# Kernel tuning notes

Hardware: AMD Instinct MI355X
Metric: run time of the kernel (lower is better)

## Reference

```python
import jax, jax.numpy as jnp
import numpy as np
from jax import lax

EPS = 1e-5


def _conv3x3(x, w):
    # NCHW input, OIHW weight, stride 1, padding 1
    return lax.conv_general_dilated(
        x, w, window_strides=(1, 1), padding=((1, 1), (1, 1)),
        dimension_numbers=("NCHW", "OIHW", "NCHW"))


def _batchnorm(y, gamma, beta):
    # training-mode BN: batch statistics over N,H,W
    mean = jnp.mean(y, axis=(0, 2, 3), keepdims=True)
    var = jnp.var(y, axis=(0, 2, 3), keepdims=True)
    inv = lax.rsqrt(var + EPS)
    return (y - mean) * inv * gamma[None, :, None, None] + beta[None, :, None, None]


def setup_inputs() -> dict:
    key = jax.random.key(0)
    k1, k2, k3 = jax.random.split(key, 3)
    N, C, H, W = 32, 128, 56, 56
    x = jax.random.normal(k1, (N, C, H, W), dtype=jnp.float32)
    w1 = jax.random.normal(k2, (C, C, 3, 3), dtype=jnp.float32) * 0.05
    w2 = jax.random.normal(k3, (C, C, 3, 3), dtype=jnp.float32) * 0.05
    gamma1 = jnp.ones((C,), jnp.float32)
    beta1 = jnp.zeros((C,), jnp.float32)
    gamma2 = jnp.ones((C,), jnp.float32)
    beta2 = jnp.zeros((C,), jnp.float32)
    return {"x": x, "w1": w1, "gamma1": gamma1, "beta1": beta1,
            "w2": w2, "gamma2": gamma2, "beta2": beta2}


def reference(x, w1, gamma1, beta1, w2, gamma2, beta2):
    # binarized conv weights: sign(w), with straight-through estimator
    # (matches torch's .data swap, which routes grads to the original weight)
    w1b = w1 + lax.stop_gradient(jnp.sign(w1) - w1)
    w2b = w2 + lax.stop_gradient(jnp.sign(w2) - w2)
    out = jax.nn.relu(_batchnorm(_conv3x3(x, w1b), gamma1, beta1))
    out = _batchnorm(_conv3x3(out, w2b), gamma2, beta2)
    out = out + x  # identity shortcut (stride=1, in_planes==planes)
    return jax.nn.relu(out)
```

## Files before the change

### kernel.cpp

```cpp
#include <hip/hip_runtime.h>

typedef unsigned short u16;
typedef unsigned short u16x8 __attribute__((ext_vector_type(8)));
typedef __bf16 bf16x8 __attribute__((ext_vector_type(8)));
typedef float f32x4 __attribute__((ext_vector_type(4)));

#define HW 3136
#define NPIX 100352
#define PADR 3364
#define KD 1152

__device__ __forceinline__ float bf2f(u16 u) {
    unsigned int x = ((unsigned int)u) << 16;
    return __builtin_bit_cast(float, x);
}
__device__ __forceinline__ u16 f2bf(float f) {
    unsigned int u = __builtin_bit_cast(unsigned int, f);
    return (u16)((u + 0x7FFFu + ((u >> 16) & 1u)) >> 16);
}
__device__ __forceinline__ void gload16(const void* g, void* l) {
    __builtin_amdgcn_global_load_lds(
        (const __attribute__((address_space(1))) unsigned int*)g,
        (__attribute__((address_space(3))) unsigned int*)l, 16, 0, 0);
}

__global__ void setup_kernel(const float* __restrict__ w1, const float* __restrict__ w2,
                             u16* __restrict__ Bm1, u16* __restrict__ Bm2,
                             u16* __restrict__ xbp) {
    const int b = blockIdx.x;
    const int t = threadIdx.x;
    if (b < 1152) {
        const float* w = (b < 576) ? w1 : w2;
        u16* Bm = (b < 576) ? Bm1 : Bm2;
        int i = (b % 576) * 256 + t;
        int k  = i / KD;
        int kk = i - k * KD;
        int c  = kk & 127;
        int rs = kk >> 7;
        float v = w[(size_t)(k * 128 + c) * 9 + rs];
        float sv = (v > 0.f) ? 1.f : ((v < 0.f) ? -1.f : 0.f);
        Bm[i] = f2bf(sv);
    } else {
        int idx = (b - 1152) * 256 + t;
        int pix = idx >> 4;
        int cc  = idx & 15;
        int n  = pix / 228;
        int pb = pix - n * 228;
        int h, w;
        if (pb < 58)       { h = 0;  w = pb; }
        else if (pb < 116) { h = 57; w = pb - 58; }
        else { int q = pb - 116; h = 1 + (q >> 1); w = (q & 1) ? 57 : 0; }
        u16x8 z = {};
        *(u16x8*)(xbp + ((size_t)(n * PADR + h * 58 + w)) * 128 + cc * 8) = z;
    }
}

__global__ void x_to_nhwc(const float* __restrict__ x, u16* __restrict__ xbp) {
    __shared__ float tile[32][65];
    const int t = threadIdx.x;
    const int n = blockIdx.y;
    const int ct = blockIdx.x & 3;
    const int pt = blockIdx.x >> 2;
    const int c0 = ct * 32, p0 = pt * 64;
    {
        const int c  = t >> 3;
        const int pw = (t & 7) * 8;
        const size_t ib = ((size_t)(n * 128 + c0 + c)) * HW + p0 + pw;
        const float4 v0 = *(const float4*)(x + ib);
        const float4 v1 = *(const float4*)(x + ib + 4);
        tile[c][pw + 0] = v0.x; tile[c][pw + 1] = v0.y;
        tile[c][pw + 2] = v0.z; tile[c][pw + 3] = v0.w;
        tile[c][pw + 4] = v1.x; tile[c][pw + 5] = v1.y;
        tile[c][pw + 6] = v1.z; tile[c][pw + 7] = v1.w;
    }
    __syncthreads();
    {
        const int pl = t >> 2;
        const int cs = (t & 3) * 8;
        const int p  = p0 + pl;
        const int h  = p / 56;
        const int w  = p - h * 56;
        u16x8 o;
#pragma unroll
        for (int j = 0; j < 8; ++j) o[j] = f2bf(tile[cs + j][pl]);
        *(u16x8*)(xbp + ((size_t)(n * PADR + (h + 1) * 58 + (w + 1))) * 128 + c0 + cs) = o;
    }
}

__global__ __launch_bounds__(256, 4) void conv_mfma(
    const u16* __restrict__ xbp, const u16* __restrict__ Bm,
    u16* __restrict__ y, float2* __restrict__ partial)
{
    __shared__ __align__(16) u16 smem[20480];
    u16* As = smem;
    u16* Bs = smem + 8192;
    const int t = threadIdx.x;
    const int bid = blockIdx.x;
    const int pm0 = bid * 128;
    const int wid  = t >> 6;
    const int lane = t & 63;
    const int lrow = lane & 15;
    const int lhk  = lane >> 4;
    const int m0 = (wid >> 1) * 64;
    const int n0 = (wid & 1) * 64;

    const int rsub = lane >> 3;
    const int csrc = (lane & 7) ^ rsub;
    int apix[4], bbase[4];
#pragma unroll
    for (int j = 0; j < 4; ++j) {
        int row = (wid * 4 + j) * 8 + rsub;
        int ps  = pm0 + row;
        int n   = ps / HW;
        int rem = ps - n * HW;
        int h   = rem / 56;
        int w   = rem - h * 56;
        apix[j]  = (n * PADR + (h + 1) * 58 + (w + 1)) * 128 + csrc * 8;
        bbase[j] = row * KD + csrc * 8;
    }

    f32x4 acc[4][4] = {};

#pragma unroll 1
    for (int pp = 0; pp < 18; ++pp) {
        const int rs_ = pp >> 1;
        const int r_ = rs_ / 3, s_ = rs_ - r_ * 3;
        const int ash = ((r_ - 1) * 58 + (s_ - 1)) * 128 + (pp & 1) * 64;
        const int bsh = pp * 64;
#pragma unroll
        for (int j = 0; j < 4; ++j) {
            gload16(xbp + apix[j] + ash, As + (wid * 4 + j) * 512);
            gload16(Bm + bbase[j] + bsh, Bs + (wid * 4 + j) * 512);
        }
        __syncthreads();
#pragma unroll
        for (int kc = 0; kc < 2; ++kc) {
            bf16x8 af[4], bv[4];
#pragma unroll
            for (int mi = 0; mi < 4; ++mi) {
                int ck = (((kc << 2) | lhk) ^ (lrow & 7)) << 3;
                af[mi] = *(const bf16x8*)&As[(m0 + mi * 16 + lrow) * 64 + ck];
            }
#pragma unroll
            for (int ni = 0; ni < 4; ++ni) {
                int ck = (((kc << 2) | lhk) ^ (lrow & 7)) << 3;
                bv[ni] = *(const bf16x8*)&Bs[(n0 + ni * 16 + lrow) * 64 + ck];
            }
#pragma unroll
            for (int mi = 0; mi < 4; ++mi)
#pragma unroll
                for (int ni = 0; ni < 4; ++ni)
                    acc[mi][ni] = __builtin_amdgcn_mfma_f32_16x16x32_bf16(
                        af[mi], bv[ni], acc[mi][ni], 0, 0, 0);
        }
        __syncthreads();
    }

    float sv[4], qv[4];
#pragma unroll
    for (int ni = 0; ni < 4; ++ni) {
        float a = 0.f, b = 0.f;
#pragma unroll
        for (int mi = 0; mi < 4; ++mi)
#pragma unroll
            for (int q = 0; q < 4; ++q) { float v = acc[mi][ni][q]; a += v; b += v * v; }
        a += __shfl_xor(a, 16); a += __shfl_xor(a, 32);
        b += __shfl_xor(b, 16); b += __shfl_xor(b, 32);
        sv[ni] = a; qv[ni] = b;
    }
    float2* sred = (float2*)(smem + 17408);
    if (lane < 16) {
#pragma unroll
        for (int ni = 0; ni < 4; ++ni)
            sred[wid * 64 + ni * 16 + lane] = make_float2(sv[ni], qv[ni]);
    }

#pragma unroll
    for (int mi = 0; mi < 4; ++mi)
#pragma unroll
        for (int ni = 0; ni < 4; ++ni)
#pragma unroll
            for (int q = 0; q < 4; ++q)
                smem[(m0 + mi * 16 + lhk * 4 + q) * 136 + n0 + ni * 16 + lrow] =
                    f2bf(acc[mi][ni][q]);
    __syncthreads();
    {
        const int px = t >> 1, half = t & 1;
        const u16* src = &smem[px * 136 + half * 64];
        u16* dst = y + (size_t)(pm0 + px) * 128 + half * 64;
#pragma unroll
        for (int j = 0; j < 8; ++j)
            *(u16x8*)(dst + j * 8) = *(const u16x8*)(src + j * 8);
    }
    if (t < 128) {
        const int ni = (t >> 4) & 3, oc = t & 15, hi = t >> 6;
        float2 u = sred[hi * 64 + ni * 16 + oc];
        float2 v = sred[(hi + 2) * 64 + ni * 16 + oc];
        partial[(size_t)t * 784 + bid] = make_float2(u.x + v.x, u.y + v.y);
    }
}

__global__ void stats_finalize(const float2* __restrict__ partial,
                               const float* __restrict__ gamma, const float* __restrict__ beta,
                               float2* __restrict__ coef) {
    __shared__ float ss[256], ss2[256];
    const int c = blockIdx.x, t = threadIdx.x;
    const float2* pc = partial + (size_t)c * 784;
    float s = 0.f, s2 = 0.f;
    for (int i = t; i < 784; i += 256) { float2 v = pc[i]; s += v.x; s2 += v.y; }
    ss[t] = s; ss2[t] = s2;
    __syncthreads();
    for (int o = 128; o > 0; o >>= 1) {
        if (t < o) { ss[t] += ss[t + o]; ss2[t] += ss2[t + o]; }
        __syncthreads();
    }
    if (t == 0) {
        double mean = (double)ss[0] / (double)NPIX;
        double var  = (double)ss2[0] / (double)NPIX - mean * mean;
        if (var < 0.0) var = 0.0;
        float inv = rsqrtf((float)var + 1e-5f);
        float a = gamma[c] * inv;
        coef[c] = make_float2(a, beta[c] - (float)mean * a);
    }
}

__global__ void bnrelu_kernel(const u16* __restrict__ y, const float2* __restrict__ coef,
                              u16* __restrict__ out1p) {
    __shared__ float2 sc[128];
    const int b = blockIdx.x;
    const int t = threadIdx.x;
    if (b >= 6272) {
        int idx = (b - 6272) * 256 + t;
        int pix = idx >> 4;
        int cc  = idx & 15;
        int n  = pix / 228;
        int pb = pix - n * 228;
        int h, w;
        if (pb < 58)       { h = 0;  w = pb; }
        else if (pb < 116) { h = 57; w = pb - 58; }
        else { int q = pb - 116; h = 1 + (q >> 1); w = (q & 1) ? 57 : 0; }
        u16x8 z = {};
        *(u16x8*)(out1p + ((size_t)(n * PADR + h * 58 + w)) * 128 + cc * 8) = z;
        return;
    }
    if (t < 128) sc[t] = coef[t];
    __syncthreads();
    size_t i = (size_t)b * 256 + t;
    u16x8 v = *(const u16x8*)(y + i * 8);
    int p  = (int)(i >> 4);
    int c0 = (int)(i & 15) * 8;
    int n   = p / HW;
    int rem = p - n * HW;
    int h   = rem / 56;
    int w   = rem - h * 56;
    u16x8 o;
#pragma unroll
    for (int j = 0; j < 8; ++j) {
        float2 k = sc[c0 + j];
        o[j] = f2bf(fmaxf(bf2f(v[j]) * k.x + k.y, 0.f));
    }
    *(u16x8*)(out1p + ((size_t)(n * PADR + (h + 1) * 58 + (w + 1))) * 128 + c0) = o;
}

__global__ void bn_add_relu_nchw(const u16* __restrict__ y2, const float2* __restrict__ coef,
                                 const u16* __restrict__ xbp, float* __restrict__ out) {
    __shared__ float tile[32][65];
    __shared__ float2 sc[32];
    const int t = threadIdx.x;
    const int n = blockIdx.y;
    const int ct = blockIdx.x & 3;
    const int pt = blockIdx.x >> 2;
    const int c0 = ct * 32, p0 = pt * 64;
    if (t < 32) sc[t] = coef[c0 + t];
    __syncthreads();
    {
        const int pl = t >> 2;
        const int cs = (t & 3) * 8;
        const int p  = p0 + pl;
        const int h  = p / 56;
        const int w  = p - h * 56;
        const u16x8 v = *(const u16x8*)(y2 + ((size_t)(n * HW + p)) * 128 + c0 + cs);
        const u16x8 xv = *(const u16x8*)(xbp +
            ((size_t)(n * PADR + (h + 1) * 58 + (w + 1))) * 128 + c0 + cs);
#pragma unroll
        for (int j = 0; j < 8; ++j) {
            float2 k = sc[cs + j];
            tile[cs + j][pl] = bf2f(v[j]) * k.x + k.y + bf2f(xv[j]);
        }
    }
    __syncthreads();
    {
        const int c  = t >> 3;
        const int pw = (t & 7) * 8;
        const size_t ob = ((size_t)(n * 128 + c0 + c)) * HW + p0 + pw;
        float4 o0, o1;
        o0.x = fmaxf(tile[c][pw + 0], 0.f);
        o0.y = fmaxf(tile[c][pw + 1], 0.f);
        o0.z = fmaxf(tile[c][pw + 2], 0.f);
        o0.w = fmaxf(tile[c][pw + 3], 0.f);
        o1.x = fmaxf(tile[c][pw + 4], 0.f);
        o1.y = fmaxf(tile[c][pw + 5], 0.f);
        o1.z = fmaxf(tile[c][pw + 6], 0.f);
        o1.w = fmaxf(tile[c][pw + 7], 0.f);
        *(float4*)(out + ob) = o0;
        *(float4*)(out + ob + 4) = o1;
    }
}

extern "C" void kernel_launch(void* const* d_in, const int* in_sizes, int n_in,
                              void* d_out, int out_size, void* d_ws, size_t ws_size,
                              hipStream_t stream) {
    const float* x  = (const float*)d_in[0];
    const float* w1 = (const float*)d_in[1];
    const float* g1 = (const float*)d_in[2];
    const float* b1 = (const float*)d_in[3];
    const float* w2 = (const float*)d_in[4];
    const float* g2 = (const float*)d_in[5];
    const float* b2 = (const float*)d_in[6];
    float* out = (float*)d_out;
    char* ws = (char*)d_ws;

    u16*    xbp   = (u16*)(ws);
    u16*    ybuf  = (u16*)(ws + 27557888);
    u16*    Bm1   = (u16*)(ws + 53248000);
    u16*    Bm2   = (u16*)(ws + 53542912);
    float2* part  = (float2*)(ws + 53837824);
    float2* cf1   = (float2*)(ws + 54640640);
    float2* cf2   = (float2*)(ws + 54641664);
    u16*    out1p = (u16*)d_out;

    setup_kernel<<<1608, 256, 0, stream>>>(w1, w2, Bm1, Bm2, xbp);
    x_to_nhwc<<<dim3(196, 32), 256, 0, stream>>>(x, xbp);

    conv_mfma<<<784, 256, 0, stream>>>(xbp, Bm1, ybuf, part);
    stats_finalize<<<128, 256, 0, stream>>>(part, g1, b1, cf1);
    bnrelu_kernel<<<6728, 256, 0, stream>>>(ybuf, cf1, out1p);

    conv_mfma<<<784, 256, 0, stream>>>(out1p, Bm2, ybuf, part);
    stats_finalize<<<128, 256, 0, stream>>>(part, g2, b2, cf2);
    bn_add_relu_nchw<<<dim3(196, 32), 256, 0, stream>>>(ybuf, cf2, xbp, out);
}
```

Measured before the change: 147.0 us.

## Merge input prep into setup kernel and remap conv block order for locality

Folds the x-to-NHWC transpose and the zeroing of out1p's padding border into the single setup kernel, which removes one kernel launch and takes the border writes out of the bnrelu kernel. The conv kernel now remaps block IDs so that consecutive launched blocks take strided pixel tiles (bid0&7 spreads blocks across XCDs), aiming at better L2 locality per chiplet. The setup kernel grows in size and now carries shared memory for every block, and the remapping changes the memory access pattern. This could help or hurt.

New measurement: 143.8 us. -2.2%, faster.

```diff
diff --git a/kernel.cpp b/kernel.cpp
--- a/kernel.cpp
+++ b/kernel.cpp
@@ -9,6 +9,7 @@
 #define NPIX 100352
 #define PADR 3364
 #define KD 1152
+#define NBLK 784
 
 __device__ __forceinline__ float bf2f(u16 u) {
     unsigned int x = ((unsigned int)u) << 16;
@@ -26,7 +27,9 @@
 
 __global__ void setup_kernel(const float* __restrict__ w1, const float* __restrict__ w2,
                              u16* __restrict__ Bm1, u16* __restrict__ Bm2,
-                             u16* __restrict__ xbp) {
+                             u16* __restrict__ xbp, u16* __restrict__ out1p,
+                             const float* __restrict__ x) {
+    __shared__ float tile[32][65];
     const int b = blockIdx.x;
     const int t = threadIdx.x;
     if (b < 1152) {
@@ -40,8 +43,12 @@
         float v = w[(size_t)(k * 128 + c) * 9 + rs];
         float sv = (v > 0.f) ? 1.f : ((v < 0.f) ? -1.f : 0.f);
         Bm[i] = f2bf(sv);
-    } else {
-        int idx = (b - 1152) * 256 + t;
+        return;
+    }
+    if (b < 2064) {
+        const bool toOut = (b >= 1608);
+        u16* dst = toOut ? out1p : xbp;
+        int idx = ((toOut ? b - 1608 : b - 1152)) * 256 + t;
         int pix = idx >> 4;
         int cc  = idx & 15;
         int n  = pix / 228;
@@ -51,39 +58,39 @@
         else if (pb < 116) { h = 57; w = pb - 58; }
         else { int q = pb - 116; h = 1 + (q >> 1); w = (q & 1) ? 57 : 0; }
         u16x8 z = {};
-        *(u16x8*)(xbp + ((size_t)(n * PADR + h * 58 + w)) * 128 + cc * 8) = z;
-    }
-}
-
-__global__ void x_to_nhwc(const float* __restrict__ x, u16* __restrict__ xbp) {
-    __shared__ float tile[32][65];
-    const int t = threadIdx.x;
-    const int n = blockIdx.y;
-    const int ct = blockIdx.x & 3;
-    const int pt = blockIdx.x >> 2;
-    const int c0 = ct * 32, p0 = pt * 64;
-    {
-        const int c  = t >> 3;
-        const int pw = (t & 7) * 8;
-        const size_t ib = ((size_t)(n * 128 + c0 + c)) * HW + p0 + pw;
-        const float4 v0 = *(const float4*)(x + ib);
-        const float4 v1 = *(const float4*)(x + ib + 4);
-        tile[c][pw + 0] = v0.x; tile[c][pw + 1] = v0.y;
-        tile[c][pw + 2] = v0.z; tile[c][pw + 3] = v0.w;
-        tile[c][pw + 4] = v1.x; tile[c][pw + 5] = v1.y;
-        tile[c][pw + 6] = v1.z; tile[c][pw + 7] = v1.w;
-    }
-    __syncthreads();
-    {
-        const int pl = t >> 2;
-        const int cs = (t & 3) * 8;
-        const int p  = p0 + pl;
-        const int h  = p / 56;
-        const int w  = p - h * 56;
-        u16x8 o;
-#pragma unroll
-        for (int j = 0; j < 8; ++j) o[j] = f2bf(tile[cs + j][pl]);
-        *(u16x8*)(xbp + ((size_t)(n * PADR + (h + 1) * 58 + (w + 1))) * 128 + c0 + cs) = o;
+        *(u16x8*)(dst + ((size_t)(n * PADR + h * 58 + w)) * 128 + cc * 8) = z;
+        return;
+    }
+    {
+        const int idx = b - 2064;
+        const int bx = idx % 196;
+        const int n  = idx / 196;
+        const int ct = bx & 3;
+        const int pt = bx >> 2;
+        const int c0 = ct * 32, p0 = pt * 64;
+        {
+            const int c  = t >> 3;
+            const int pw = (t & 7) * 8;
+            const size_t ib = ((size_t)(n * 128 + c0 + c)) * HW + p0 + pw;
+            const float4 v0 = *(const float4*)(x + ib);
+            const float4 v1 = *(const float4*)(x + ib + 4);
+            tile[c][pw + 0] = v0.x; tile[c][pw + 1] = v0.y;
+            tile[c][pw + 2] = v0.z; tile[c][pw + 3] = v0.w;
+            tile[c][pw + 4] = v1.x; tile[c][pw + 5] = v1.y;
+            tile[c][pw + 6] = v1.z; tile[c][pw + 7] = v1.w;
+        }
+        __syncthreads();
+        {
+            const int pl = t >> 2;
+            const int cs = (t & 3) * 8;
+            const int p  = p0 + pl;
+            const int h  = p / 56;
+            const int w  = p - h * 56;
+            u16x8 o;
+#pragma unroll
+            for (int j = 0; j < 8; ++j) o[j] = f2bf(tile[cs + j][pl]);
+            *(u16x8*)(xbp + ((size_t)(n * PADR + (h + 1) * 58 + (w + 1))) * 128 + c0 + cs) = o;
+        }
     }
 }
 
@@ -95,7 +102,8 @@
     u16* As = smem;
     u16* Bs = smem + 8192;
     const int t = threadIdx.x;
-    const int bid = blockIdx.x;
+    const int bid0 = blockIdx.x;
+    const int bid = (bid0 & 7) * 98 + (bid0 >> 3);
     const int pm0 = bid * 128;
     const int wid  = t >> 6;
     const int lane = t & 63;
@@ -156,23 +164,25 @@
         __syncthreads();
     }
 
-    float sv[4], qv[4];
-#pragma unroll
-    for (int ni = 0; ni < 4; ++ni) {
-        float a = 0.f, b = 0.f;
-#pragma unroll
-        for (int mi = 0; mi < 4; ++mi)
-#pragma unroll
-            for (int q = 0; q < 4; ++q) { float v = acc[mi][ni][q]; a += v; b += v * v; }
-        a += __shfl_xor(a, 16); a += __shfl_xor(a, 32);
-        b += __shfl_xor(b, 16); b += __shfl_xor(b, 32);
-        sv[ni] = a; qv[ni] = b;
-    }
     float2* sred = (float2*)(smem + 17408);
-    if (lane < 16) {
-#pragma unroll
-        for (int ni = 0; ni < 4; ++ni)
-            sred[wid * 64 + ni * 16 + lane] = make_float2(sv[ni], qv[ni]);
+    {
+        float sv[4], qv[4];
+#pragma unroll
+        for (int ni = 0; ni < 4; ++ni) {
+            float a = 0.f, b = 0.f;
+#pragma unroll
+            for (int mi = 0; mi < 4; ++mi)
+#pragma unroll
+                for (int q = 0; q < 4; ++q) { float v = acc[mi][ni][q]; a += v; b += v * v; }
+            a += __shfl_xor(a, 16); a += __shfl_xor(a, 32);
+            b += __shfl_xor(b, 16); b += __shfl_xor(b, 32);
+            sv[ni] = a; qv[ni] = b;
+        }
+        if (lane < 16) {
+#pragma unroll
+            for (int ni = 0; ni < 4; ++ni)
+                sred[wid * 64 + ni * 16 + lane] = make_float2(sv[ni], qv[ni]);
+        }
     }
 
 #pragma unroll
@@ -196,7 +206,7 @@
         const int ni = (t >> 4) & 3, oc = t & 15, hi = t >> 6;
         float2 u = sred[hi * 64 + ni * 16 + oc];
         float2 v = sred[(hi + 2) * 64 + ni * 16 + oc];
-        partial[(size_t)t * 784 + bid] = make_float2(u.x + v.x, u.y + v.y);
+        partial[(size_t)t * NBLK + bid] = make_float2(u.x + v.x, u.y + v.y);
     }
 }
 
@@ -205,9 +215,9 @@
                                float2* __restrict__ coef) {
     __shared__ float ss[256], ss2[256];
     const int c = blockIdx.x, t = threadIdx.x;
-    const float2* pc = partial + (size_t)c * 784;
+    const float2* pc = partial + (size_t)c * NBLK;
     float s = 0.f, s2 = 0.f;
-    for (int i = t; i < 784; i += 256) { float2 v = pc[i]; s += v.x; s2 += v.y; }
+    for (int i = t; i < NBLK; i += 256) { float2 v = pc[i]; s += v.x; s2 += v.y; }
     ss[t] = s; ss2[t] = s2;
     __syncthreads();
     for (int o = 128; o > 0; o >>= 1) {
@@ -227,25 +237,10 @@
 __global__ void bnrelu_kernel(const u16* __restrict__ y, const float2* __restrict__ coef,
                               u16* __restrict__ out1p) {
     __shared__ float2 sc[128];
-    const int b = blockIdx.x;
     const int t = threadIdx.x;
-    if (b >= 6272) {
-        int idx = (b - 6272) * 256 + t;
-        int pix = idx >> 4;
-        int cc  = idx & 15;
-        int n  = pix / 228;
-        int pb = pix - n * 228;
-        int h, w;
-        if (pb < 58)       { h = 0;  w = pb; }
-        else if (pb < 116) { h = 57; w = pb - 58; }
-        else { int q = pb - 116; h = 1 + (q >> 1); w = (q & 1) ? 57 : 0; }
-        u16x8 z = {};
-        *(u16x8*)(out1p + ((size_t)(n * PADR + h * 58 + w)) * 128 + cc * 8) = z;
-        return;
-    }
     if (t < 128) sc[t] = coef[t];
     __syncthreads();
-    size_t i = (size_t)b * 256 + t;
+    size_t i = (size_t)blockIdx.x * 256 + t;
     u16x8 v = *(const u16x8*)(y + i * 8);
     int p  = (int)(i >> 4);
     int c0 = (int)(i & 15) * 8;
@@ -329,14 +324,13 @@
     float2* cf2   = (float2*)(ws + 54641664);
     u16*    out1p = (u16*)d_out;
 
-    setup_kernel<<<1608, 256, 0, stream>>>(w1, w2, Bm1, Bm2, xbp);
-    x_to_nhwc<<<dim3(196, 32), 256, 0, stream>>>(x, xbp);
-
-    conv_mfma<<<784, 256, 0, stream>>>(xbp, Bm1, ybuf, part);
+    setup_kernel<<<8336, 256, 0, stream>>>(w1, w2, Bm1, Bm2, xbp, out1p, x);
+
+    conv_mfma<<<NBLK, 256, 0, stream>>>(xbp, Bm1, ybuf, part);
     stats_finalize<<<128, 256, 0, stream>>>(part, g1, b1, cf1);
-    bnrelu_kernel<<<6728, 256, 0, stream>>>(ybuf, cf1, out1p);
-
-    conv_mfma<<<784, 256, 0, stream>>>(out1p, Bm2, ybuf, part);
+    bnrelu_kernel<<<6272, 256, 0, stream>>>(ybuf, cf1, out1p);
+
+    conv_mfma<<<NBLK, 256, 0, stream>>>(out1p, Bm2, ybuf, part);
     stats_finalize<<<128, 256, 0, stream>>>(part, g2, b2, cf2);
     bn_add_relu_nchw<<<dim3(196, 32), 256, 0, stream>>>(ybuf, cf2, xbp, out);
 }
```
